# Kernel optimization log

Hardware: AMD Instinct MI355X
Metric: run time of the kernel (lower is better)

## Reference

```python
import jax, jax.numpy as jnp
import numpy as np

HEADS = 4
NEG_SLOPE = 0.2  # PyG GATConv default
LN_EPS = 1e-5


def setup_inputs() -> dict:
    key = jax.random.key(0)
    ks = jax.random.split(key, 12)
    N, D, E = 30000, 128, 480000
    s = 1.0 / np.sqrt(D)
    return {
        "x": jax.random.normal(ks[0], (N, D), dtype=jnp.float32),
        "edge_index": jax.random.randint(ks[1], (2, E), 0, N, dtype=jnp.int64),
        "W_gat": jax.random.normal(ks[2], (HEADS, D, D), dtype=jnp.float32) * s,
        "att_src": jax.random.normal(ks[3], (HEADS, D), dtype=jnp.float32) * s,
        "att_dst": jax.random.normal(ks[4], (HEADS, D), dtype=jnp.float32) * s,
        "b_gat": jnp.zeros((D,), dtype=jnp.float32),
        "W_gcn": jax.random.normal(ks[5], (D, D), dtype=jnp.float32) * s,
        "b_gcn": jnp.zeros((D,), dtype=jnp.float32),
        "W_gate": jax.random.normal(ks[6], (2 * D, 2), dtype=jnp.float32) * (1.0 / np.sqrt(2 * D)),
        "b_gate": jnp.zeros((2,), dtype=jnp.float32),
        "gamma": jnp.ones((D,), dtype=jnp.float32),
        "beta": jnp.zeros((D,), dtype=jnp.float32),
    }


def reference(x, edge_index, W_gat, att_src, att_dst, b_gat, W_gcn, b_gcn,
              W_gate, b_gate, gamma, beta):
    N, D = x.shape
    # Both PyG GATConv and GCNConv add self-loops by default.
    loops = jnp.arange(N, dtype=edge_index.dtype)
    src = jnp.concatenate([edge_index[0], loops])  # message source j
    dst = jnp.concatenate([edge_index[1], loops])  # message target i

    # ---- GATConv (heads=4, concat=False -> mean over heads), eval (no dropout) ----
    xh = jnp.einsum('nd,hdf->nhf', x, W_gat)            # [N, H, D]
    a_s = jnp.einsum('nhf,hf->nh', xh, att_src)         # [N, H]
    a_d = jnp.einsum('nhf,hf->nh', xh, att_dst)         # [N, H]
    e = jax.nn.leaky_relu(a_s[src] + a_d[dst], NEG_SLOPE)  # [E', H]
    # segment softmax over incoming edges of each destination node
    m = jax.ops.segment_max(e, dst, num_segments=N)     # every node has a self-loop
    alpha = jnp.exp(e - m[dst])
    denom = jax.ops.segment_sum(alpha, dst, num_segments=N)
    alpha = alpha / denom[dst]                          # [E', H]
    # aggregate per head (fixed small loop keeps peak memory at E*D per head)
    gat_acc = jnp.zeros((N, D), dtype=x.dtype)
    for h in range(HEADS):
        msg = alpha[:, h:h + 1] * xh[:, h, :][src]      # [E', D]
        gat_acc = gat_acc + jax.ops.segment_sum(msg, dst, num_segments=N)
    gat_out = gat_acc / HEADS + b_gat

    xg = x @ W_gcn                                      # [N, D]
    deg = jax.ops.segment_sum(jnp.ones_like(src, dtype=x.dtype), dst, num_segments=N)
    dinv = jnp.where(deg > 0, jax.lax.rsqrt(deg), 0.0)
    coef = dinv[src] * dinv[dst]                        # [E']
    gcn_out = jax.ops.segment_sum(coef[:, None] * xg[src], dst, num_segments=N) + b_gcn

    # ---- gated fusion + residual + LayerNorm ----
    gate = jax.nn.softmax(jnp.concatenate([gat_out, gcn_out], axis=-1) @ W_gate + b_gate, axis=-1)
    fused = gate[:, 0:1] * gat_out + gate[:, 1:2] * gcn_out
    h = fused + gat_out
    mu = jnp.mean(h, axis=-1, keepdims=True)
    var = jnp.mean((h - mu) ** 2, axis=-1, keepdims=True)
    return (h - mu) * jax.lax.rsqrt(var + LN_EPS) * gamma + beta
```

## Files before the change

kernel.cpp:

```cpp
#include <hip/hip_runtime.h>
#include <hip/hip_bf16.h>

#define D 128
#define NH 4
#define NEG_SLOPE 0.2f
#define LN_EPS 1e-5f

typedef __attribute__((ext_vector_type(4))) float f32x4;
typedef __attribute__((ext_vector_type(8))) short bf16x8;

__device__ __forceinline__ float bf2f(unsigned short u) {
  union { unsigned int i; float f; } c; c.i = ((unsigned int)u) << 16; return c.f;
}
__device__ __forceinline__ unsigned short f2bf(float f) {
  union { float f; unsigned int i; } c; c.f = f;
  unsigned int r = c.i + 0x7FFFu + ((c.i >> 16) & 1u);
  return (unsigned short)(r >> 16);
}

__global__ __launch_bounds__(128) void k_prep(
    const float* __restrict__ Wgat, const float* __restrict__ Wgcn,
    const float* __restrict__ att_src, const float* __restrict__ att_dst,
    unsigned short* __restrict__ Wt2g, unsigned short* __restrict__ Wt2c,
    float* __restrict__ wtil_s, float* __restrict__ wtil_d,
    int* __restrict__ deg, int N)
{
  int c = blockIdx.x, t = threadIdx.x;
  if (c < 128) {
    #pragma unroll
    for (int i = 0; i < 4; ++i) {
      int k = t + i * 128;
      int h = k >> 7, kk = k & 127;
      Wt2g[c * 512 + k] = f2bf(Wgat[((size_t)h * D + kk) * D + c]);
    }
  } else if (c < 256) {
    int cc = c - 128;
    Wt2c[cc * 128 + t] = f2bf(Wgcn[(size_t)t * D + cc]);
  } else if (c < 264) {
    int b2 = c - 256;
    int h = b2 >> 1, which = b2 & 1;
    const float* av = (which ? att_dst : att_src) + h * D;
    const float* Wrow = Wgat + ((size_t)h * D + t) * D;
    float s = 0.f;
    for (int f = 0; f < D; ++f) s += Wrow[f] * av[f];
    (which ? wtil_d : wtil_s)[h * D + t] = s;
  } else {
    int i = (c - 264) * 128 + t;
    if (i < N) deg[i] = 0;
  }
}

__global__ __launch_bounds__(256) void k_xb_deg(
    const float* __restrict__ x,
    const float* __restrict__ wtil_s, const float* __restrict__ wtil_d,
    unsigned short* __restrict__ xb, float* __restrict__ a_s, float* __restrict__ a_d,
    const int* __restrict__ ei, int* __restrict__ deg,
    int N, int E, int NBN)
{
  if ((int)blockIdx.x >= NBN) {
    int e = (blockIdx.x - NBN) * 256 + threadIdx.x;
    if (e < E + N) {
      int dst = (e < E) ? ei[E + e] : (e - E);
      atomicAdd(&deg[dst], 1);
    }
    return;
  }
  const int w = threadIdx.x >> 6, l = threadIdx.x & 63;
  const int n = blockIdx.x * 4 + w;
  if (n >= N) return;
  float2 xv = ((const float2*)(x + (size_t)n * D))[l];
  ushort2 p; p.x = f2bf(xv.x); p.y = f2bf(xv.y);
  *(ushort2*)(xb + (size_t)n * D + 2 * l) = p;
  float s0 = xv.x * wtil_s[2*l]       + xv.y * wtil_s[2*l+1];
  float s1 = xv.x * wtil_s[D+2*l]     + xv.y * wtil_s[D+2*l+1];
  float s2 = xv.x * wtil_s[2*D+2*l]   + xv.y * wtil_s[2*D+2*l+1];
  float s3 = xv.x * wtil_s[3*D+2*l]   + xv.y * wtil_s[3*D+2*l+1];
  float d0 = xv.x * wtil_d[2*l]       + xv.y * wtil_d[2*l+1];
  float d1 = xv.x * wtil_d[D+2*l]     + xv.y * wtil_d[D+2*l+1];
  float d2 = xv.x * wtil_d[2*D+2*l]   + xv.y * wtil_d[2*D+2*l+1];
  float d3 = xv.x * wtil_d[3*D+2*l]   + xv.y * wtil_d[3*D+2*l+1];
  #pragma unroll
  for (int off = 32; off; off >>= 1) {
    s0 += __shfl_xor(s0, off); s1 += __shfl_xor(s1, off);
    s2 += __shfl_xor(s2, off); s3 += __shfl_xor(s3, off);
    d0 += __shfl_xor(d0, off); d1 += __shfl_xor(d1, off);
    d2 += __shfl_xor(d2, off); d3 += __shfl_xor(d3, off);
  }
  if (l == 0) {
    ((float4*)a_s)[n] = make_float4(s0, s1, s2, s3);
    ((float4*)a_d)[n] = make_float4(d0, d1, d2, d3);
  }
}

__global__ void k_scan1(const int* __restrict__ deg, int N, int* __restrict__ bsum)
{
  __shared__ int s[256];
  int t = threadIdx.x;
  int i = blockIdx.x * 256 + t;
  s[t] = (i < N) ? deg[i] : 0;
  __syncthreads();
  for (int off = 128; off; off >>= 1) {
    if (t < off) s[t] += s[t + off];
    __syncthreads();
  }
  if (t == 0) bsum[blockIdx.x] = s[0];
}

__global__ void k_scan2(int* __restrict__ bsum, int nb)
{
  __shared__ int s[128];
  int t = threadIdx.x;
  int v = (t < nb) ? bsum[t] : 0;
  s[t] = v; __syncthreads();
  for (int off = 1; off < 128; off <<= 1) {
    int xv = (t >= off) ? s[t - off] : 0;
    __syncthreads();
    s[t] += xv;
    __syncthreads();
  }
  if (t < nb) bsum[t] = s[t] - v;
}

__global__ void k_scan3(const int* __restrict__ deg, const int* __restrict__ bsum,
                        int N, int Et, int* __restrict__ row_ptr,
                        int* __restrict__ cursor, float* __restrict__ dinv)
{
  __shared__ int s[256];
  int t = threadIdx.x;
  int i = blockIdx.x * 256 + t;
  int v = (i < N) ? deg[i] : 0;
  s[t] = v; __syncthreads();
  for (int off = 1; off < 256; off <<= 1) {
    int xv = (t >= off) ? s[t - off] : 0;
    __syncthreads();
    s[t] += xv;
    __syncthreads();
  }
  if (i < N) {
    int excl = s[t] - v + bsum[blockIdx.x];
    row_ptr[i] = excl;
    cursor[i] = excl;
    dinv[i] = rsqrtf((float)v);
  }
  if (i == 0) row_ptr[N] = Et;
}

__global__ void k_fill(const int* __restrict__ ei, int E, int N,
                       int* __restrict__ cursor, int* __restrict__ col_src)
{
  int e = blockIdx.x * blockDim.x + threadIdx.x;
  if (e >= E + N) return;
  int src, dst;
  if (e < E) { src = ei[e]; dst = ei[E + e]; }
  else       { src = e - E; dst = src; }
  int pos = atomicAdd(&cursor[dst], 1);
  col_src[pos] = src;
}

__global__ __launch_bounds__(256) void k_agg2(
    const unsigned short* __restrict__ xb,
    const float* __restrict__ a_s, const float* __restrict__ a_d,
    const int* __restrict__ row_ptr, const int* __restrict__ col_src,
    const float* __restrict__ dinv,
    unsigned short* __restrict__ UV, int N)
{
  __shared__ float4 sh_al[8][33];
  __shared__ int    sh_src[8][33];
  __shared__ float  sh_cf[8][33];
  const int hw = threadIdx.x >> 5, lh = threadIdx.x & 31;
  const int n = blockIdx.x * 8 + hw;
  if (n >= N) return;
  const int start = row_ptr[n], end = row_ptr[n + 1];
  const float4 adn = ((const float4*)a_d)[n];

  float den0 = 0.f, den1 = 0.f, den2 = 0.f, den3 = 0.f;
  float ug[4][4] = {};
  float vg[4] = {};

  for (int base = start; base < end; base += 32) {
    const int cnt = min(32, end - base);
    if (lh < cnt) {
      int s = col_src[base + lh];
      float4 as4 = ((const float4*)a_s)[s];
      float e0 = as4.x + adn.x; e0 = (e0 >= 0.f) ? e0 : NEG_SLOPE * e0;
      float e1 = as4.y + adn.y; e1 = (e1 >= 0.f) ? e1 : NEG_SLOPE * e1;
      float e2 = as4.z + adn.z; e2 = (e2 >= 0.f) ? e2 : NEG_SLOPE * e2;
      float e3 = as4.w + adn.w; e3 = (e3 >= 0.f) ? e3 : NEG_SLOPE * e3;
      float x0 = __expf(e0), x1 = __expf(e1), x2 = __expf(e2), x3 = __expf(e3);
      den0 += x0; den1 += x1; den2 += x2; den3 += x3;
      sh_al[hw][lh] = make_float4(x0, x1, x2, x3);
      sh_src[hw][lh] = s;
      sh_cf[hw][lh] = dinv[s];
    }
    if (lh == 0) {
      sh_al[hw][cnt] = make_float4(0.f, 0.f, 0.f, 0.f);
      sh_src[hw][cnt] = 0;
      sh_cf[hw][cnt] = 0.f;
    }
    for (int j = 0; j < cnt; j += 2) {
      float4 alA = sh_al[hw][j];     int sA = sh_src[hw][j];     float cfA = sh_cf[hw][j];
      float4 alB = sh_al[hw][j + 1]; int sB = sh_src[hw][j + 1]; float cfB = sh_cf[hw][j + 1];
      ushort4 xA = *(const ushort4*)(xb + ((size_t)sA << 7) + (lh << 2));
      ushort4 xB = *(const ushort4*)(xb + ((size_t)sB << 7) + (lh << 2));
      float fa[4] = {bf2f(xA.x), bf2f(xA.y), bf2f(xA.z), bf2f(xA.w)};
      float fb[4] = {bf2f(xB.x), bf2f(xB.y), bf2f(xB.z), bf2f(xB.w)};
      float aA[4] = {alA.x, alA.y, alA.z, alA.w};
      float aB[4] = {alB.x, alB.y, alB.z, alB.w};
      #pragma unroll
      for (int h = 0; h < 4; ++h)
        #pragma unroll
        for (int d = 0; d < 4; ++d)
          ug[h][d] += aA[h] * fa[d] + aB[h] * fb[d];
      #pragma unroll
      for (int d = 0; d < 4; ++d)
        vg[d] += cfA * fa[d] + cfB * fb[d];
    }
  }

  #pragma unroll
  for (int off = 16; off; off >>= 1) {
    den0 += __shfl_xor(den0, off); den1 += __shfl_xor(den1, off);
    den2 += __shfl_xor(den2, off); den3 += __shfl_xor(den3, off);
  }
  const float r[4] = {1.f / den0, 1.f / den1, 1.f / den2, 1.f / den3};
  const float dn = dinv[n];
  unsigned short* uvp = UV + (size_t)n * 640;
  #pragma unroll
  for (int h = 0; h < 4; ++h) {
    ushort4 u;
    u.x = f2bf(ug[h][0] * r[h]); u.y = f2bf(ug[h][1] * r[h]);
    u.z = f2bf(ug[h][2] * r[h]); u.w = f2bf(ug[h][3] * r[h]);
    *(ushort4*)(uvp + h * 128 + 4 * lh) = u;
  }
  ushort4 v4;
  v4.x = f2bf(vg[0] * dn); v4.y = f2bf(vg[1] * dn);
  v4.z = f2bf(vg[2] * dn); v4.w = f2bf(vg[3] * dn);
  *(ushort4*)(uvp + 512 + 4 * lh) = v4;
}

__global__ __launch_bounds__(256) void k_gemm3(
    const unsigned short* __restrict__ UV,
    const unsigned short* __restrict__ Wt2g, const unsigned short* __restrict__ Wt2c,
    const float* __restrict__ b_gat, const float* __restrict__ b_gcn,
    const float* __restrict__ W_gate, const float* __restrict__ b_gate,
    const float* __restrict__ gamma, const float* __restrict__ beta,
    float* __restrict__ out, int N)
{
  __shared__ unsigned short As[64 * 128];
  __shared__ unsigned short Bs[128 * 128];
  __shared__ float ec[8][128];
  const int t = threadIdx.x;
  const int m0 = blockIdx.x * 64;

  {
    int idx = t * 4;
    #pragma unroll
    for (int i = 0; i < 4; ++i) {
      int arr = (idx + i) >> 7, c = (idx + i) & 127;
      float v;
      switch (arr) {
        case 0: v = b_gat[c]; break;
        case 1: v = b_gcn[c]; break;
        case 2: v = W_gate[2 * c]; break;
        case 3: v = W_gate[2 * c + 1]; break;
        case 4: v = W_gate[256 + 2 * c]; break;
        case 5: v = W_gate[256 + 2 * c + 1]; break;
        case 6: v = gamma[c]; break;
        default: v = beta[c]; break;
      }
      ec[arr][c] = v;
    }
  }

  const int w = t >> 6, l = t & 63;
  const int lrow = l & 15, lk = l >> 4;
  const int arow = w * 16 + lrow;

  f32x4 accg[8], accc[8];
  #pragma unroll
  for (int n = 0; n < 8; ++n) {
    accg[n] = (f32x4){0.f, 0.f, 0.f, 0.f};
    accc[n] = (f32x4){0.f, 0.f, 0.f, 0.f};
  }

  for (int kc = 0; kc < 5; ++kc) {
    const int abase = (kc < 4) ? kc * 128 : 512;
    __syncthreads();
    #pragma unroll
    for (int i = 0; i < 4; ++i) {
      int g = i * 256 + t;
      int row = g >> 4, kb = g & 15;
      int gr = m0 + row;
      uint4 v = make_uint4(0u, 0u, 0u, 0u);
      if (gr < N) v = *(const uint4*)(UV + (size_t)gr * 640 + abase + kb * 8);
      *(uint4*)&As[row * 128 + ((kb ^ (row & 7)) << 3)] = v;
    }
    #pragma unroll
    for (int i = 0; i < 8; ++i) {
      int g = i * 256 + t;
      int col = g >> 4, kb = g & 15;
      uint4 v = (kc < 4)
        ? *(const uint4*)(Wt2g + (size_t)col * 512 + kc * 128 + kb * 8)
        : *(const uint4*)(Wt2c + (size_t)col * 128 + kb * 8);
      *(uint4*)&Bs[col * 128 + ((kb ^ (col & 7)) << 3)] = v;
    }
    __syncthreads();
    f32x4* acc = (kc < 4) ? accg : accc;
    #pragma unroll
    for (int ks = 0; ks < 4; ++ks) {
      int kb = ks * 4 + lk;
      bf16x8 a = *(const bf16x8*)&As[arow * 128 + ((kb ^ (arow & 7)) << 3)];
      #pragma unroll
      for (int n = 0; n < 8; ++n) {
        int col = n * 16 + lrow;
        bf16x8 b = *(const bf16x8*)&Bs[col * 128 + ((kb ^ (col & 7)) << 3)];
        acc[n] = __builtin_amdgcn_mfma_f32_16x16x32_bf16(a, b, acc[n], 0, 0, 0);
      }
    }
  }

  const float bg0 = b_gate[0], bg1 = b_gate[1];
  #pragma unroll
  for (int j = 0; j < 4; ++j) {
    const int r = m0 + w * 16 + lk * 4 + j;
    float ga[8], gc[8];
    float z0 = 0.f, z1 = 0.f;
    #pragma unroll
    for (int n = 0; n < 8; ++n) {
      int c = n * 16 + lrow;
      ga[n] = accg[n][j] * 0.25f + ec[0][c];
      gc[n] = accc[n][j] + ec[1][c];
      z0 += ga[n] * ec[2][c] + gc[n] * ec[4][c];
      z1 += ga[n] * ec[3][c] + gc[n] * ec[5][c];
    }
    #pragma unroll
    for (int off = 8; off; off >>= 1) { z0 += __shfl_xor(z0, off); z1 += __shfl_xor(z1, off); }
    z0 += bg0; z1 += bg1;
    float mz = fmaxf(z0, z1);
    float e0 = __expf(z0 - mz), e1 = __expf(z1 - mz);
    float inv = 1.f / (e0 + e1);
    float w0 = e0 * inv, w1 = e1 * inv;
    float h[8], ss = 0.f;
    #pragma unroll
    for (int n = 0; n < 8; ++n) { h[n] = (1.f + w0) * ga[n] + w1 * gc[n]; ss += h[n]; }
    #pragma unroll
    for (int off = 8; off; off >>= 1) ss += __shfl_xor(ss, off);
    float mu = ss * (1.f / 128.f);
    float vs = 0.f;
    #pragma unroll
    for (int n = 0; n < 8; ++n) { h[n] -= mu; vs += h[n] * h[n]; }
    #pragma unroll
    for (int off = 8; off; off >>= 1) vs += __shfl_xor(vs, off);
    float rstd = rsqrtf(vs * (1.f / 128.f) + LN_EPS);
    if (r < N) {
      #pragma unroll
      for (int n = 0; n < 8; ++n) {
        int c = n * 16 + lrow;
        out[(size_t)r * 128 + c] = h[n] * rstd * ec[6][c] + ec[7][c];
      }
    }
  }
}

extern "C" void kernel_launch(void* const* d_in, const int* in_sizes, int n_in,
                              void* d_out, int out_size, void* d_ws, size_t ws_size,
                              hipStream_t stream)
{
  const float* x       = (const float*)d_in[0];
  const int*   ei      = (const int*)d_in[1];
  const float* Wgat    = (const float*)d_in[2];
  const float* att_src = (const float*)d_in[3];
  const float* att_dst = (const float*)d_in[4];
  const float* b_gat   = (const float*)d_in[5];
  const float* Wgcn    = (const float*)d_in[6];
  const float* b_gcn   = (const float*)d_in[7];
  const float* W_gate  = (const float*)d_in[8];
  const float* b_gate  = (const float*)d_in[9];
  const float* gamma   = (const float*)d_in[10];
  const float* beta    = (const float*)d_in[11];
  float* out = (float*)d_out;

  const int N  = in_sizes[0] / D;
  const int E  = in_sizes[1] / 2;
  const int Et = E + N;

  char* p = (char*)d_ws;
  unsigned short* xb   = (unsigned short*)p; p += (size_t)N * D * 2;
  unsigned short* UV   = (unsigned short*)p; p += (size_t)N * 640 * 2;
  unsigned short* Wt2g = (unsigned short*)p; p += (size_t)128 * 512 * 2;
  unsigned short* Wt2c = (unsigned short*)p; p += (size_t)128 * 128 * 2;
  float* wtil_s  = (float*)p; p += 512 * 4;
  float* wtil_d  = (float*)p; p += 512 * 4;
  float* a_s     = (float*)p; p += (size_t)N * NH * 4;
  float* a_d     = (float*)p; p += (size_t)N * NH * 4;
  float* dinv    = (float*)p; p += (size_t)N * 4;
  int* deg       = (int*)p;   p += (size_t)N * 4;
  int* row_ptr   = (int*)p;   p += (size_t)(N + 1) * 4;
  int* cursor    = (int*)p;   p += (size_t)N * 4;
  int* col_src   = (int*)p;   p += (size_t)Et * 4;
  int* bsum      = (int*)p;   p += 1024;

  const int NBN = (N + 3) / 4;
  const int NBE = (Et + 255) / 256;

  k_prep<<<264 + (N + 127) / 128, 128, 0, stream>>>(
      Wgat, Wgcn, att_src, att_dst, Wt2g, Wt2c, wtil_s, wtil_d, deg, N);
  k_xb_deg<<<NBN + NBE, 256, 0, stream>>>(x, wtil_s, wtil_d, xb, a_s, a_d,
                                           ei, deg, N, E, NBN);
  int nb = (N + 255) / 256;
  k_scan1<<<nb, 256, 0, stream>>>(deg, N, bsum);
  k_scan2<<<1, 128, 0, stream>>>(bsum, nb);
  k_scan3<<<nb, 256, 0, stream>>>(deg, bsum, N, Et, row_ptr, cursor, dinv);
  k_fill<<<(Et + 255) / 256, 256, 0, stream>>>(ei, E, N, cursor, col_src);
  k_agg2<<<(N + 7) / 8, 256, 0, stream>>>(xb, a_s, a_d, row_ptr, col_src, dinv, UV, N);
  k_gemm3<<<(N + 63) / 64, 256, 0, stream>>>(UV, Wt2g, Wt2c, b_gat, b_gcn,
                                              W_gate, b_gate, gamma, beta, out, N);
  (void)n_in; (void)out_size; (void)ws_size;
}
```

Before: 131.9 us.

## Fuse three-pass degree scan into single-pass decoupled scan; nontemporal UV/out accesses

Replaces the three scan kernels (block sums, scan of sums, final scan) with one kernel. Each block publishes its total to a zeroed partial array, then spin-waits on all earlier blocks' totals and reduces them to get its base offset. This removes two kernel launches. The spin-wait assumes all 118 blocks can be resident at once, which holds on this GPU. Separately, the UV stores in aggregation and the UV loads and output stores in the GEMM become nontemporal, to reduce cache pollution.

Measured after the change: 138.4 us. +4.9%, slower.

```diff
diff --git a/kernel.cpp b/kernel.cpp
--- a/kernel.cpp
+++ b/kernel.cpp
@@ -8,6 +8,8 @@
 
 typedef __attribute__((ext_vector_type(4))) float f32x4;
 typedef __attribute__((ext_vector_type(8))) short bf16x8;
+typedef __attribute__((ext_vector_type(2))) unsigned int u32x2;
+typedef __attribute__((ext_vector_type(4))) unsigned int u32x4;
 
 __device__ __forceinline__ float bf2f(unsigned short u) {
   union { unsigned int i; float f; } c; c.i = ((unsigned int)u) << 16; return c.f;
@@ -23,7 +25,7 @@
     const float* __restrict__ att_src, const float* __restrict__ att_dst,
     unsigned short* __restrict__ Wt2g, unsigned short* __restrict__ Wt2c,
     float* __restrict__ wtil_s, float* __restrict__ wtil_d,
-    int* __restrict__ deg, int N)
+    int* __restrict__ deg, int* __restrict__ partial, int N, int nzb)
 {
   int c = blockIdx.x, t = threadIdx.x;
   if (c < 128) {
@@ -44,9 +46,11 @@
     float s = 0.f;
     for (int f = 0; f < D; ++f) s += Wrow[f] * av[f];
     (which ? wtil_d : wtil_s)[h * D + t] = s;
-  } else {
+  } else if (c < 264 + nzb) {
     int i = (c - 264) * 128 + t;
     if (i < N) deg[i] = 0;
+  } else {
+    if (t < 256) partial[t] = 0;
   }
 }
 
@@ -92,43 +96,16 @@
   }
 }
 
-__global__ void k_scan1(const int* __restrict__ deg, int N, int* __restrict__ bsum)
+__global__ __launch_bounds__(256) void k_scan(
+    const int* __restrict__ deg, int N, int Et,
+    int* __restrict__ row_ptr, int* __restrict__ cursor, float* __restrict__ dinv,
+    int* __restrict__ partial)
 {
   __shared__ int s[256];
-  int t = threadIdx.x;
-  int i = blockIdx.x * 256 + t;
-  s[t] = (i < N) ? deg[i] : 0;
-  __syncthreads();
-  for (int off = 128; off; off >>= 1) {
-    if (t < off) s[t] += s[t + off];
-    __syncthreads();
-  }
-  if (t == 0) bsum[blockIdx.x] = s[0];
-}
-
-__global__ void k_scan2(int* __restrict__ bsum, int nb)
-{
-  __shared__ int s[128];
-  int t = threadIdx.x;
-  int v = (t < nb) ? bsum[t] : 0;
-  s[t] = v; __syncthreads();
-  for (int off = 1; off < 128; off <<= 1) {
-    int xv = (t >= off) ? s[t - off] : 0;
-    __syncthreads();
-    s[t] += xv;
-    __syncthreads();
-  }
-  if (t < nb) bsum[t] = s[t] - v;
-}
-
-__global__ void k_scan3(const int* __restrict__ deg, const int* __restrict__ bsum,
-                        int N, int Et, int* __restrict__ row_ptr,
-                        int* __restrict__ cursor, float* __restrict__ dinv)
-{
-  __shared__ int s[256];
-  int t = threadIdx.x;
-  int i = blockIdx.x * 256 + t;
-  int v = (i < N) ? deg[i] : 0;
+  __shared__ int r[256];
+  const int t = threadIdx.x, b = blockIdx.x;
+  const int i = b * 256 + t;
+  const int v = (i < N) ? deg[i] : 0;
   s[t] = v; __syncthreads();
   for (int off = 1; off < 256; off <<= 1) {
     int xv = (t >= off) ? s[t - off] : 0;
@@ -136,8 +113,25 @@
     s[t] += xv;
     __syncthreads();
   }
+  if (t == 0)
+    __hip_atomic_store(&partial[b], s[255] + 1, __ATOMIC_RELEASE, __HIP_MEMORY_SCOPE_AGENT);
+  int pv = 0;
+  if (t < b) {
+    int p;
+    do {
+      p = __hip_atomic_load(&partial[t], __ATOMIC_ACQUIRE, __HIP_MEMORY_SCOPE_AGENT);
+      if (p == 0) __builtin_amdgcn_s_sleep(2);
+    } while (p == 0);
+    pv = p - 1;
+  }
+  r[t] = pv; __syncthreads();
+  for (int off = 128; off; off >>= 1) {
+    if (t < off) r[t] += r[t + off];
+    __syncthreads();
+  }
+  const int base = r[0];
   if (i < N) {
-    int excl = s[t] - v + bsum[blockIdx.x];
+    int excl = base + s[t] - v;
     row_ptr[i] = excl;
     cursor[i] = excl;
     dinv[i] = rsqrtf((float)v);
@@ -227,15 +221,15 @@
   unsigned short* uvp = UV + (size_t)n * 640;
   #pragma unroll
   for (int h = 0; h < 4; ++h) {
-    ushort4 u;
-    u.x = f2bf(ug[h][0] * r[h]); u.y = f2bf(ug[h][1] * r[h]);
-    u.z = f2bf(ug[h][2] * r[h]); u.w = f2bf(ug[h][3] * r[h]);
-    *(ushort4*)(uvp + h * 128 + 4 * lh) = u;
-  }
-  ushort4 v4;
-  v4.x = f2bf(vg[0] * dn); v4.y = f2bf(vg[1] * dn);
-  v4.z = f2bf(vg[2] * dn); v4.w = f2bf(vg[3] * dn);
-  *(ushort4*)(uvp + 512 + 4 * lh) = v4;
+    u32x2 u;
+    u.x = (unsigned int)f2bf(ug[h][0] * r[h]) | ((unsigned int)f2bf(ug[h][1] * r[h]) << 16);
+    u.y = (unsigned int)f2bf(ug[h][2] * r[h]) | ((unsigned int)f2bf(ug[h][3] * r[h]) << 16);
+    __builtin_nontemporal_store(u, (u32x2*)(uvp + h * 128 + 4 * lh));
+  }
+  u32x2 v2;
+  v2.x = (unsigned int)f2bf(vg[0] * dn) | ((unsigned int)f2bf(vg[1] * dn) << 16);
+  v2.y = (unsigned int)f2bf(vg[2] * dn) | ((unsigned int)f2bf(vg[3] * dn) << 16);
+  __builtin_nontemporal_store(v2, (u32x2*)(uvp + 512 + 4 * lh));
 }
 
 __global__ __launch_bounds__(256) void k_gemm3(
@@ -291,9 +285,9 @@
       int g = i * 256 + t;
       int row = g >> 4, kb = g & 15;
       int gr = m0 + row;
-      uint4 v = make_uint4(0u, 0u, 0u, 0u);
-      if (gr < N) v = *(const uint4*)(UV + (size_t)gr * 640 + abase + kb * 8);
-      *(uint4*)&As[row * 128 + ((kb ^ (row & 7)) << 3)] = v;
+      u32x4 v = (u32x4){0u, 0u, 0u, 0u};
+      if (gr < N) v = __builtin_nontemporal_load((const u32x4*)(UV + (size_t)gr * 640 + abase + kb * 8));
+      *(u32x4*)&As[row * 128 + ((kb ^ (row & 7)) << 3)] = v;
     }
     #pragma unroll
     for (int i = 0; i < 8; ++i) {
@@ -356,7 +350,8 @@
       #pragma unroll
       for (int n = 0; n < 8; ++n) {
         int c = n * 16 + lrow;
-        out[(size_t)r * 128 + c] = h[n] * rstd * ec[6][c] + ec[7][c];
+        __builtin_nontemporal_store(h[n] * rstd * ec[6][c] + ec[7][c],
+                                    out + (size_t)r * 128 + c);
       }
     }
   }
@@ -398,20 +393,19 @@
   int* row_ptr   = (int*)p;   p += (size_t)(N + 1) * 4;
   int* cursor    = (int*)p;   p += (size_t)N * 4;
   int* col_src   = (int*)p;   p += (size_t)Et * 4;
-  int* bsum      = (int*)p;   p += 1024;
+  int* partial   = (int*)p;   p += 1024;
 
   const int NBN = (N + 3) / 4;
   const int NBE = (Et + 255) / 256;
-
-  k_prep<<<264 + (N + 127) / 128, 128, 0, stream>>>(
-      Wgat, Wgcn, att_src, att_dst, Wt2g, Wt2c, wtil_s, wtil_d, deg, N);
+  const int nzb = (N + 127) / 128;
+  const int nb  = (N + 255) / 256;
+
+  k_prep<<<264 + nzb + 1, 128, 0, stream>>>(
+      Wgat, Wgcn, att_src, att_dst, Wt2g, Wt2c, wtil_s, wtil_d, deg, partial, N, nzb);
   k_xb_deg<<<NBN + NBE, 256, 0, stream>>>(x, wtil_s, wtil_d, xb, a_s, a_d,
                                            ei, deg, N, E, NBN);
-  int nb = (N + 255) / 256;
-  k_scan1<<<nb, 256, 0, stream>>>(deg, N, bsum);
-  k_scan2<<<1, 128, 0, stream>>>(bsum, nb);
-  k_scan3<<<nb, 256, 0, stream>>>(deg, bsum, N, Et, row_ptr, cursor, dinv);
-  k_fill<<<(Et + 255) / 256, 256, 0, stream>>>(ei, E, N, cursor, col_src);
+  k_scan<<<nb, 256, 0, stream>>>(deg, N, Et, row_ptr, cursor, dinv, partial);
+  k_fill<<<NBE, 256, 0, stream>>>(ei, E, N, cursor, col_src);
   k_agg2<<<(N + 7) / 8, 256, 0, stream>>>(xb, a_s, a_d, row_ptr, col_src, dinv, UV, N);
   k_gemm3<<<(N + 63) / 64, 256, 0, stream>>>(UV, Wt2g, Wt2c, b_gat, b_gcn,
                                               W_gate, b_gate, gamma, beta, out, N);
```
